# Performance work log

Measured on AMD Instinct MI355X. Metric: run time of the kernel, lower is better.

Reference implementation:

```python
import jax, jax.numpy as jnp
import numpy as np

N_NODES = 50000
N_EDGES = 800000
N_FEAT = 128
N_GRAPHS = 512
OUT_DIM = 128


def gcn_conv(x, W, b, src, dst, ew, n):
    """PyG GCNConv: h = x @ W; add self-loops (weight 1); symmetric norm
    D^-1/2 A D^-1/2 with edge weights; scatter-add messages src->dst; + bias."""
    h = x @ W  # [n, out]
    loop = jnp.arange(n)
    s = jnp.concatenate([src, loop])
    d = jnp.concatenate([dst, loop])
    w = jnp.concatenate([ew, jnp.ones((n,), x.dtype)])
    deg = jax.ops.segment_sum(w, d, num_segments=n)
    dinv = jnp.where(deg > 0, jax.lax.rsqrt(deg), 0.0)
    norm = dinv[s] * w * dinv[d]  # [E+n]
    out = jax.ops.segment_sum(h[s] * norm[:, None], d, num_segments=n)
    return out + b


def setup_inputs() -> dict:
    key = jax.random.key(0)
    ks = jax.random.split(key, 12)
    F = N_FEAT
    x = jax.random.normal(ks[0], (N_NODES, F), jnp.float32)
    edge_index = jax.random.randint(ks[1], (2, N_EDGES), 0, N_NODES, jnp.int64)
    edge_attr = jax.random.uniform(ks[2], (N_EDGES,), jnp.float32)
    # deterministic sorted graph assignment -> no empty graphs (avoids -inf in max pool)
    batch = (jnp.arange(N_NODES, dtype=jnp.int64) * N_GRAPHS) // N_NODES
    def lin(k, fi, fo):
        s = 1.0 / np.sqrt(fi)
        return jax.random.uniform(k, (fi, fo), jnp.float32, -s, s)
    return {
        "x": x, "edge_attr": edge_attr,
        "W1": lin(ks[3], F, F), "b1": jnp.zeros((F,), jnp.float32),
        "W2": lin(ks[4], F, 2 * F), "b2": jnp.zeros((2 * F,), jnp.float32),
        "W3": lin(ks[5], 2 * F, 4 * F), "b3": jnp.zeros((4 * F,), jnp.float32),
        "Wf1": lin(ks[6], 4 * F, 1024), "bf1": jnp.zeros((1024,), jnp.float32),
        "Wf2": lin(ks[7], 1024, OUT_DIM), "bf2": jnp.zeros((OUT_DIM,), jnp.float32),
        "edge_index": edge_index, "batch": batch,
    }


def reference(x, edge_attr, W1, b1, W2, b2, W3, b3, Wf1, bf1, Wf2, bf2,
              edge_index, batch):
    n = x.shape[0]
    src, dst = edge_index[0], edge_index[1]
    h = jax.nn.relu(gcn_conv(x, W1, b1, src, dst, edge_attr, n))
    h = jax.nn.relu(gcn_conv(h, W2, b2, src, dst, edge_attr, n))
    h = jax.nn.relu(gcn_conv(h, W3, b3, src, dst, edge_attr, n))
    # global max pool over nodes per graph
    g = jax.ops.segment_max(h, batch, num_segments=N_GRAPHS)  # [G, 4F]
    g = jax.nn.relu(g @ Wf1 + bf1)
    # dropout is identity in eval mode
    out = g @ Wf2 + bf2
    return out
```

## Files before the change

kernel.cpp:

```cpp
#include <hip/hip_runtime.h>

#define NNODES 50000
#define NPAD   50048
#define NEDGES 800000
#define NGRAPH 512
#define DCAP 64

typedef short bf16x8 __attribute__((ext_vector_type(8)));
typedef unsigned short u16x8 __attribute__((ext_vector_type(8)));
typedef float f32x4 __attribute__((ext_vector_type(4)));
typedef unsigned long long u64;

#define GLOAD16(g, l)                                                                 \
    __builtin_amdgcn_global_load_lds((const __attribute__((address_space(1))) unsigned*)(g), \
                                     (__attribute__((address_space(3))) unsigned*)(l), 16, 0, 0)

static __device__ __forceinline__ float b2f(unsigned short u) {
    return __uint_as_float(((unsigned)u) << 16);
}
static __device__ __forceinline__ unsigned short f2b(float f) {
    unsigned u = __float_as_uint(f);
    unsigned r = (u + 0x7fffu + ((u >> 16) & 1u)) >> 16;
    return (unsigned short)r;
}

static __device__ __forceinline__ void accum8(float (&acc)[8], float c, uint4 v) {
    unsigned w[4] = {v.x, v.y, v.z, v.w};
    #pragma unroll
    for (int i = 0; i < 4; ++i) {
        acc[2 * i]     += c * __uint_as_float(w[i] << 16);
        acc[2 * i + 1] += c * __uint_as_float(w[i] & 0xffff0000u);
    }
}

__global__ __launch_bounds__(256) void k_init(const float* __restrict__ W1, const float* __restrict__ W2,
                                              const float* __restrict__ W3, const float* __restrict__ Wf1,
                                              const float* __restrict__ Wf2,
                                              unsigned short* __restrict__ T1, unsigned short* __restrict__ T2,
                                              unsigned short* __restrict__ T3, unsigned short* __restrict__ Tf1,
                                              unsigned short* __restrict__ Tf2,
                                              u64* deg_cnt, int* gp) {
    int i = blockIdx.x * 256 + threadIdx.x;
    if (i < NNODES) deg_cnt[i] = (u64)(1u << 24);
    if (i < NGRAPH * 512) gp[i] = 0;

    const int b = blockIdx.x;
    if (b >= 204) return;
    const float* W; unsigned short* T; int K, N, t0;
    if (b < 4)        { W = W1;  T = T1;  K = 128;  N = 128;  t0 = 0;   }
    else if (b < 12)  { W = W2;  T = T2;  K = 128;  N = 256;  t0 = 4;   }
    else if (b < 44)  { W = W3;  T = T3;  K = 256;  N = 512;  t0 = 12;  }
    else if (b < 172) { W = Wf1; T = Tf1; K = 512;  N = 1024; t0 = 44;  }
    else              { W = Wf2; T = Tf2; K = 1024; N = 128;  t0 = 172; }
    const int tile = b - t0;
    const int ntn = N >> 6;
    const int k0 = (tile / ntn) * 64, n0 = (tile % ntn) * 64;
    __shared__ float sm[64][65];
    const int t = threadIdx.x;
    const int rr = t >> 6, cc = t & 63;
    #pragma unroll
    for (int r = 0; r < 16; ++r) {
        int kl = r * 4 + rr;
        sm[kl][cc] = W[(size_t)(k0 + kl) * N + n0 + cc];
    }
    __syncthreads();
    #pragma unroll
    for (int r = 0; r < 16; ++r) {
        int nl = r * 4 + rr;
        T[(size_t)(n0 + nl) * K + k0 + cc] = f2b(sm[cc][nl]);
    }
}

__global__ __launch_bounds__(256) void k_count(const int4* __restrict__ ei_s,
                                               const int4* __restrict__ ei_d,
                                               const float4* __restrict__ ew4,
                                               u64* deg_cnt,
                                               unsigned* __restrict__ edges) {
    int t = blockIdx.x * 256 + threadIdx.x;
    if (t >= NEDGES / 4) return;
    int4 ss = ei_s[t];
    int4 dd = ei_d[t];
    float4 ww = ew4[t];
    int s[4] = {ss.x, ss.y, ss.z, ss.w};
    int d[4] = {dd.x, dd.y, dd.z, dd.w};
    float w[4] = {ww.x, ww.y, ww.z, ww.w};
    int slot[4];
    #pragma unroll
    for (int u = 0; u < 4; ++u) {
        unsigned fixed = __float2uint_rn(w[u] * 16777216.0f);
        u64 old = atomicAdd(&deg_cnt[d[u]], ((u64)1 << 32) | fixed);
        slot[u] = (int)(old >> 32);
        if (slot[u] > DCAP - 1) slot[u] = DCAP - 1;
    }
    #pragma unroll
    for (int u = 0; u < 4; ++u)
        edges[((unsigned)d[u] << 6) | slot[u]] = ((unsigned)f2b(w[u]) << 16) | (unsigned)s[u];
}

__global__ void k_cvt_prep(const float* __restrict__ X, const u64* __restrict__ deg_cnt,
                           float* __restrict__ dinv, unsigned short* __restrict__ Y, int n4) {
    int i = blockIdx.x * 256 + threadIdx.x;
    if (i < n4) {
        int row = i >> 5;
        float d = rsqrtf((float)(unsigned)(deg_cnt[row] & 0xffffffffull) * 5.9604645e-8f);
        if ((i & 31) == 0) dinv[row] = d;
        float4 v = ((const float4*)X)[i];
        uint2 o;
        o.x = (unsigned)f2b(v.x * d) | ((unsigned)f2b(v.y * d) << 16);
        o.y = (unsigned)f2b(v.z * d) | ((unsigned)f2b(v.w * d) << 16);
        ((uint2*)Y)[i] = o;
    }
}

template <int F, int SLICES>
__global__ __launch_bounds__(256) void k_aggregate(const unsigned short* __restrict__ X,
                                                   const u64* __restrict__ deg_cnt,
                                                   const unsigned* __restrict__ edges,
                                                   const float* __restrict__ dinv,
                                                   unsigned short* __restrict__ Z) {
    constexpr int FS = F / SLICES;
    constexpr int LPR = FS / 8;
    constexpr int GRP = 64 / LPR;
    constexpr int STEP = GRP * 2;
    const int bid = blockIdx.x;
    const int slice = (SLICES == 1) ? 0 : (bid & (SLICES - 1));
    const int chunk = (SLICES == 1) ? bid : (bid / SLICES);
    const int wave = threadIdx.x >> 6, lane = threadIdx.x & 63;
    const int node = chunk * 4 + wave;
    if (node >= NNODES) return;
    const int sub = lane & (LPR - 1);
    const int grp = lane / LPR;
    const int fo = slice * FS + sub * 8;
    const unsigned short* Xf = X + fo;
    const float di = dinv[node];
    const int cnt = (int)(deg_cnt[node] >> 32);
    const unsigned* erow = edges + ((unsigned)node << 6);

    const uint4 selfv = *(const uint4*)(Xf + (size_t)node * F);

    float acc[8] = {};

    const int e0 = grp;
    const int nb = (cnt + STEP - 1) / STEP;

    unsigned pa0 = 0, pb0 = 0, pa1 = 0, pb1 = 0;
    uint4 va0 = {}, vb0 = {};
    if (nb > 0) {
        int ea = e0, eb = e0 + GRP;
        pa0 = (ea < cnt) ? erow[ea] : 0u;
        pb0 = (eb < cnt) ? erow[eb] : 0u;
        va0 = *(const uint4*)(Xf + (size_t)(pa0 & 0xffffu) * F);
        vb0 = *(const uint4*)(Xf + (size_t)(pb0 & 0xffffu) * F);
        if (nb > 1) {
            int ea1 = e0 + STEP, eb1 = ea1 + GRP;
            pa1 = (ea1 < cnt) ? erow[ea1] : 0u;
            pb1 = (eb1 < cnt) ? erow[eb1] : 0u;
        }
    }
    for (int p = 0; p < nb; ++p) {
        uint4 va1 = {}, vb1 = {};
        unsigned pa2 = 0, pb2 = 0;
        if (p + 1 < nb) {
            va1 = *(const uint4*)(Xf + (size_t)(pa1 & 0xffffu) * F);
            vb1 = *(const uint4*)(Xf + (size_t)(pb1 & 0xffffu) * F);
            if (p + 2 < nb) {
                int ea = e0 + (p + 2) * STEP, eb = ea + GRP;
                pa2 = (ea < cnt) ? erow[ea] : 0u;
                pb2 = (eb < cnt) ? erow[eb] : 0u;
            }
        }
        accum8(acc, b2f((unsigned short)(pa0 >> 16)), va0);
        accum8(acc, b2f((unsigned short)(pb0 >> 16)), vb0);
        pa0 = pa1; pb0 = pb1; va0 = va1; vb0 = vb1;
        pa1 = pa2; pb1 = pb2;
    }

    #pragma unroll
    for (int j = 0; j < 8; ++j) {
        if constexpr (GRP == 4) acc[j] += __shfl_xor(acc[j], 16, 64);
        acc[j] += __shfl_xor(acc[j], 32, 64);
    }

    if (grp == 0) {
        unsigned w[4] = {selfv.x, selfv.y, selfv.z, selfv.w};
        unsigned o[4];
        #pragma unroll
        for (int i = 0; i < 4; ++i) {
            float s0 = __uint_as_float(w[i] << 16);
            float s1 = __uint_as_float(w[i] & 0xffff0000u);
            unsigned short c0 = f2b(di * (acc[2 * i] + s0));
            unsigned short c1 = f2b(di * (acc[2 * i + 1] + s1));
            o[i] = (unsigned)c0 | ((unsigned)c1 << 16);
        }
        uint4 ov; ov.x = o[0]; ov.y = o[1]; ov.z = o[2]; ov.w = o[3];
        *(uint4*)(Z + (size_t)node * F + fo) = ov;
    }
}

template <int CMODE>
__global__ __launch_bounds__(256) void k_gemm128(const unsigned short* __restrict__ A,
                                                 const unsigned short* __restrict__ WT,
                                                 const float* __restrict__ bias,
                                                 unsigned short* __restrict__ C,
                                                 const int* __restrict__ batch,
                                                 int* __restrict__ gp,
                                                 const float* __restrict__ rscale,
                                                 int M, int N, int K) {
    __shared__ unsigned short As[2][128 * 32];
    __shared__ unsigned short Bs[2][128 * 32];
    const int tid = threadIdx.x;

    const int nwg = gridDim.x * gridDim.y;
    const int f = blockIdx.y * gridDim.x + blockIdx.x;
    const int q = nwg >> 3, r = nwg & 7;
    const int xcd = f & 7, idx = f >> 3;
    const int w = (xcd < r) ? xcd * (q + 1) + idx : r * (q + 1) + (xcd - r) * q + idx;
    const int m0 = (w / gridDim.x) * 128;
    const int n0 = (w % gridDim.x) * 128;

    const int wave = tid >> 6, lane = tid & 63;
    const int wm = (wave >> 1) * 64, wn = (wave & 1) * 64;
    const int quad = lane >> 4, mrow = lane & 15;

    const int sr = tid >> 2;
    const int sc = (tid & 3) * 8;
    const unsigned short* Ag0 = A + (size_t)(m0 + sr) * K + sc;
    const unsigned short* Ag1 = A + (size_t)(m0 + 64 + sr) * K + sc;
    const unsigned short* Bg0 = WT + (size_t)(n0 + sr) * K + sc;
    const unsigned short* Bg1 = WT + (size_t)(n0 + 64 + sr) * K + sc;
    const int so0 = sr * 32 + sc, so1 = (64 + sr) * 32 + sc;

    f32x4 acc[4][4] = {};
    const int nsteps = K >> 5;

    GLOAD16(Ag0, &As[0][so0]);
    GLOAD16(Ag1, &As[0][so1]);
    GLOAD16(Bg0, &Bs[0][so0]);
    GLOAD16(Bg1, &Bs[0][so1]);
    __syncthreads();

    for (int step = 0; step < nsteps; ++step) {
        const int cur = step & 1;
        if (step + 1 < nsteps) {
            const int k1 = (step + 1) << 5;
            GLOAD16(Ag0 + k1, &As[cur ^ 1][so0]);
            GLOAD16(Ag1 + k1, &As[cur ^ 1][so1]);
            GLOAD16(Bg0 + k1, &Bs[cur ^ 1][so0]);
            GLOAD16(Bg1 + k1, &Bs[cur ^ 1][so1]);
        }
        bf16x8 af[4], bf[4];
        #pragma unroll
        for (int mt = 0; mt < 4; ++mt)
            af[mt] = *(const bf16x8*)&As[cur][(wm + mt * 16 + mrow) * 32 + quad * 8];
        #pragma unroll
        for (int nt = 0; nt < 4; ++nt)
            bf[nt] = *(const bf16x8*)&Bs[cur][(wn + nt * 16 + mrow) * 32 + quad * 8];
        #pragma unroll
        for (int mt = 0; mt < 4; ++mt)
            #pragma unroll
            for (int nt = 0; nt < 4; ++nt)
                acc[mt][nt] = __builtin_amdgcn_mfma_f32_16x16x32_bf16(af[mt], bf[nt], acc[mt][nt], 0, 0, 0);
        __syncthreads();
    }

    float bn[4];
    #pragma unroll
    for (int nt = 0; nt < 4; ++nt) bn[nt] = bias[n0 + wn + nt * 16 + mrow];

    if constexpr (CMODE == 0) {
        #pragma unroll
        for (int mt = 0; mt < 4; ++mt) {
            #pragma unroll
            for (int r4 = 0; r4 < 4; ++r4) {
                int row = m0 + wm + mt * 16 + quad * 4 + r4;
                if (row < M) {
                    float rs = rscale ? rscale[row] : 1.0f;
                    #pragma unroll
                    for (int nt = 0; nt < 4; ++nt) {
                        float v = fmaxf(acc[mt][nt][r4] + bn[nt], 0.f) * rs;
                        C[(size_t)row * N + n0 + wn + nt * 16 + mrow] = f2b(v);
                    }
                }
            }
        }
    } else {
        const int wr0 = m0 + wm;
        int g0i = wr0 < M ? wr0 : M - 1;
        const int g0 = batch[g0i];
        int lastr = wr0 + 63; if (lastr >= M) lastr = M - 1;
        const int gl = batch[lastr];
        bool rok[16]; int gid[16];
        #pragma unroll
        for (int mt = 0; mt < 4; ++mt)
            #pragma unroll
            for (int r4 = 0; r4 < 4; ++r4) {
                int row = wr0 + mt * 16 + quad * 4 + r4;
                rok[mt * 4 + r4] = row < M;
                gid[mt * 4 + r4] = (row < M) ? batch[row] : -1;
            }
        #pragma unroll
        for (int nt = 0; nt < 4; ++nt) {
            float v0 = 0.f, v1 = 0.f;
            #pragma unroll
            for (int mt = 0; mt < 4; ++mt)
                #pragma unroll
                for (int r4 = 0; r4 < 4; ++r4)
                    if (rok[mt * 4 + r4]) {
                        float v = fmaxf(acc[mt][nt][r4] + bn[nt], 0.f);
                        if (gid[mt * 4 + r4] == g0) v0 = fmaxf(v0, v);
                        else v1 = fmaxf(v1, v);
                    }
            v0 = fmaxf(v0, __shfl_xor(v0, 16, 64));
            v0 = fmaxf(v0, __shfl_xor(v0, 32, 64));
            v1 = fmaxf(v1, __shfl_xor(v1, 16, 64));
            v1 = fmaxf(v1, __shfl_xor(v1, 32, 64));
            if (quad == 0) {
                int c = n0 + wn + nt * 16 + mrow;
                atomicMax(&gp[(size_t)g0 * N + c], __float_as_int(v0));
                if (gl != g0) atomicMax(&gp[(size_t)gl * N + c], __float_as_int(v1));
            }
        }
    }
}

template <int CMODE, int AFP>
__global__ __launch_bounds__(256) void k_gemm_mfma(const void* __restrict__ Av,
                                                   const unsigned short* __restrict__ WT,
                                                   const float* __restrict__ bias,
                                                   void* __restrict__ Cv,
                                                   int M, int N, int K) {
    constexpr int LDK = 40;
    __shared__ unsigned short As[64 * LDK];
    __shared__ unsigned short Bs[128 * LDK];
    const int tid = threadIdx.x;
    const int m0 = blockIdx.y * 64, n0 = blockIdx.x * 128;
    const int wave = tid >> 6, lane = tid & 63;
    const int wm = (wave >> 1) * 32;
    const int wn = (wave & 1) * 64;
    const int quad = lane >> 4, mrow = lane & 15;

    const int ar = tid >> 2;
    const int ak = (tid & 3) * 8;
    const bool arow_ok = (m0 + ar) < M;
    const size_t aoff = (size_t)(m0 + ar) * K + ak;
    const unsigned short* Bg0 = WT + (size_t)(n0 + ar) * K + ak;
    const unsigned short* Bg1 = WT + (size_t)(n0 + ar + 64) * K + ak;

    f32x4 acc[2][4] = {};

    for (int k0 = 0; k0 < K; k0 += 32) {
        u16x8 av = {};
        if (arow_ok) {
            if constexpr (AFP) {
                const float* Af = (const float*)Av + aoff + k0;
                float4 f0 = *(const float4*)Af;
                float4 f1 = *(const float4*)(Af + 4);
                av[0] = (short)f2b(f0.x); av[1] = (short)f2b(f0.y);
                av[2] = (short)f2b(f0.z); av[3] = (short)f2b(f0.w);
                av[4] = (short)f2b(f1.x); av[5] = (short)f2b(f1.y);
                av[6] = (short)f2b(f1.z); av[7] = (short)f2b(f1.w);
            } else {
                av = *(const u16x8*)((const unsigned short*)Av + aoff + k0);
            }
        }
        u16x8 bv0 = *(const u16x8*)(Bg0 + k0);
        u16x8 bv1 = *(const u16x8*)(Bg1 + k0);
        *(u16x8*)&As[ar * LDK + ak] = av;
        *(u16x8*)&Bs[ar * LDK + ak] = bv0;
        *(u16x8*)&Bs[(ar + 64) * LDK + ak] = bv1;
        __syncthreads();
        bf16x8 af[2], bf[4];
        #pragma unroll
        for (int mt = 0; mt < 2; ++mt)
            af[mt] = *(const bf16x8*)&As[(wm + mt * 16 + mrow) * LDK + quad * 8];
        #pragma unroll
        for (int nt = 0; nt < 4; ++nt)
            bf[nt] = *(const bf16x8*)&Bs[(wn + nt * 16 + mrow) * LDK + quad * 8];
        #pragma unroll
        for (int mt = 0; mt < 2; ++mt)
            #pragma unroll
            for (int nt = 0; nt < 4; ++nt)
                acc[mt][nt] = __builtin_amdgcn_mfma_f32_16x16x32_bf16(af[mt], bf[nt], acc[mt][nt], 0, 0, 0);
        __syncthreads();
    }

    float bn[4];
    #pragma unroll
    for (int nt = 0; nt < 4; ++nt) bn[nt] = bias[n0 + wn + nt * 16 + mrow];

    if constexpr (CMODE == 0) {
        unsigned short* C = (unsigned short*)Cv;
        #pragma unroll
        for (int mt = 0; mt < 2; ++mt) {
            #pragma unroll
            for (int r = 0; r < 4; ++r) {
                int row = m0 + wm + mt * 16 + quad * 4 + r;
                if (row < M) {
                    #pragma unroll
                    for (int nt = 0; nt < 4; ++nt) {
                        float v = fmaxf(acc[mt][nt][r] + bn[nt], 0.f);
                        C[(size_t)row * N + n0 + wn + nt * 16 + mrow] = f2b(v);
                    }
                }
            }
        }
    } else {
        float* C = (float*)Cv;
        #pragma unroll
        for (int mt = 0; mt < 2; ++mt) {
            #pragma unroll
            for (int r = 0; r < 4; ++r) {
                int row = m0 + wm + mt * 16 + quad * 4 + r;
                if (row < M) {
                    #pragma unroll
                    for (int nt = 0; nt < 4; ++nt)
                        C[(size_t)row * N + n0 + wn + nt * 16 + mrow] = acc[mt][nt][r] + bn[nt];
                }
            }
        }
    }
}

extern "C" void kernel_launch(void* const* d_in, const int* in_sizes, int n_in,
                              void* d_out, int out_size, void* d_ws, size_t ws_size,
                              hipStream_t stream) {
    const float* x   = (const float*)d_in[0];
    const float* ew  = (const float*)d_in[1];
    const float* W1  = (const float*)d_in[2];
    const float* b1  = (const float*)d_in[3];
    const float* W2  = (const float*)d_in[4];
    const float* b2  = (const float*)d_in[5];
    const float* W3  = (const float*)d_in[6];
    const float* b3  = (const float*)d_in[7];
    const float* Wf1 = (const float*)d_in[8];
    const float* bf1 = (const float*)d_in[9];
    const float* Wf2 = (const float*)d_in[10];
    const float* bf2 = (const float*)d_in[11];
    const int* ei    = (const int*)d_in[12];
    const int* batch = (const int*)d_in[13];
    float* out = (float*)d_out;
    (void)in_sizes; (void)n_in; (void)out_size; (void)ws_size;

    char* p = (char*)d_ws;
    auto alloc = [&](size_t bytes) -> char* {
        char* r = p;
        p += (bytes + 255) & ~(size_t)255;
        return r;
    };
    u64*   deg_cnt = (u64*)alloc((size_t)NNODES * 8);
    float* dinv   = (float*)alloc((size_t)NNODES * 4);
    unsigned* edges = (unsigned*)alloc((size_t)NNODES * DCAP * 4);
    int*   gp     = (int*)  alloc((size_t)NGRAPH * 512 * 4);
    unsigned short* f1   = (unsigned short*)alloc((size_t)NGRAPH * 1024 * 2);
    unsigned short* wt1  = (unsigned short*)alloc((size_t)128 * 128 * 2);
    unsigned short* wt2  = (unsigned short*)alloc((size_t)256 * 128 * 2);
    unsigned short* wt3  = (unsigned short*)alloc((size_t)512 * 256 * 2);
    unsigned short* wtf1 = (unsigned short*)alloc((size_t)1024 * 512 * 2);
    unsigned short* wtf2 = (unsigned short*)alloc((size_t)128 * 1024 * 2);
    unsigned short* bufA = (unsigned short*)alloc((size_t)NPAD * 256 * 2);
    unsigned short* bufB = (unsigned short*)alloc((size_t)NPAD * 256 * 2);
    unsigned short* x16  = bufB;

    const int MB128 = (NNODES + 127) / 128;
    const int AGG = (NNODES + 3) / 4;

    k_init<<<1024, 256, 0, stream>>>(W1, W2, W3, Wf1, Wf2,
                                     wt1, wt2, wt3, wtf1, wtf2, deg_cnt, gp);
    k_count<<<(NEDGES / 4 + 255) / 256, 256, 0, stream>>>(
        (const int4*)ei, (const int4*)(ei + NEDGES), (const float4*)ew, deg_cnt, edges);
    k_cvt_prep<<<(NNODES * 32 + 255) / 256, 256, 0, stream>>>(x, deg_cnt, dinv, x16, NNODES * 32);

    k_aggregate<128, 1><<<AGG, 256, 0, stream>>>(x16, deg_cnt, edges, dinv, bufA);
    k_gemm128<0><<<dim3(1, MB128), 256, 0, stream>>>(bufA, wt1, b1, bufB, nullptr, nullptr, dinv, NNODES, 128, 128);
    k_aggregate<128, 1><<<AGG, 256, 0, stream>>>(bufB, deg_cnt, edges, dinv, bufA);
    k_gemm128<0><<<dim3(2, MB128), 256, 0, stream>>>(bufA, wt2, b2, bufB, nullptr, nullptr, dinv, NNODES, 256, 128);
    k_aggregate<256, 2><<<AGG * 2, 256, 0, stream>>>(bufB, deg_cnt, edges, dinv, bufA);
    k_gemm128<2><<<dim3(4, MB128), 256, 0, stream>>>(bufA, wt3, b3, nullptr, batch, gp, nullptr, NNODES, 512, 256);

    k_gemm_mfma<0, 1><<<dim3(8, NGRAPH / 64), 256, 0, stream>>>(gp, wtf1, bf1, f1, NGRAPH, 1024, 512);
    k_gemm_mfma<1, 0><<<dim3(1, NGRAPH / 64), 256, 0, stream>>>(f1, wtf2, bf2, out, NGRAPH, 128, 1024);
}
```

Baseline: 363.6 us.

## Merge weight transpose and edge bucketing into one kernel, pad degree counters

```diff
diff --git a/kernel.cpp b/kernel.cpp
--- a/kernel.cpp
+++ b/kernel.cpp
@@ -33,68 +33,52 @@
     }
 }
 
-__global__ __launch_bounds__(256) void k_init(const float* __restrict__ W1, const float* __restrict__ W2,
-                                              const float* __restrict__ W3, const float* __restrict__ Wf1,
-                                              const float* __restrict__ Wf2,
-                                              unsigned short* __restrict__ T1, unsigned short* __restrict__ T2,
-                                              unsigned short* __restrict__ T3, unsigned short* __restrict__ Tf1,
-                                              unsigned short* __restrict__ Tf2,
-                                              u64* deg_cnt, int* gp) {
-    int i = blockIdx.x * 256 + threadIdx.x;
-    if (i < NNODES) deg_cnt[i] = (u64)(1u << 24);
-    if (i < NGRAPH * 512) gp[i] = 0;
-
+__global__ __launch_bounds__(256) void k_graph(const float* __restrict__ W1, const float* __restrict__ W2,
+                                               const float* __restrict__ W3, const float* __restrict__ Wf1,
+                                               const float* __restrict__ Wf2,
+                                               unsigned short* __restrict__ T1, unsigned short* __restrict__ T2,
+                                               unsigned short* __restrict__ T3, unsigned short* __restrict__ Tf1,
+                                               unsigned short* __restrict__ Tf2,
+                                               const int* __restrict__ ei_s, const int* __restrict__ ei_d,
+                                               const float* __restrict__ ew,
+                                               u64* deg_cnt, unsigned* __restrict__ edges) {
     const int b = blockIdx.x;
-    if (b >= 204) return;
-    const float* W; unsigned short* T; int K, N, t0;
-    if (b < 4)        { W = W1;  T = T1;  K = 128;  N = 128;  t0 = 0;   }
-    else if (b < 12)  { W = W2;  T = T2;  K = 128;  N = 256;  t0 = 4;   }
-    else if (b < 44)  { W = W3;  T = T3;  K = 256;  N = 512;  t0 = 12;  }
-    else if (b < 172) { W = Wf1; T = Tf1; K = 512;  N = 1024; t0 = 44;  }
-    else              { W = Wf2; T = Tf2; K = 1024; N = 128;  t0 = 172; }
-    const int tile = b - t0;
-    const int ntn = N >> 6;
-    const int k0 = (tile / ntn) * 64, n0 = (tile % ntn) * 64;
-    __shared__ float sm[64][65];
-    const int t = threadIdx.x;
-    const int rr = t >> 6, cc = t & 63;
-    #pragma unroll
-    for (int r = 0; r < 16; ++r) {
-        int kl = r * 4 + rr;
-        sm[kl][cc] = W[(size_t)(k0 + kl) * N + n0 + cc];
-    }
-    __syncthreads();
-    #pragma unroll
-    for (int r = 0; r < 16; ++r) {
-        int nl = r * 4 + rr;
-        T[(size_t)(n0 + nl) * K + k0 + cc] = f2b(sm[cc][nl]);
-    }
-}
-
-__global__ __launch_bounds__(256) void k_count(const int4* __restrict__ ei_s,
-                                               const int4* __restrict__ ei_d,
-                                               const float4* __restrict__ ew4,
-                                               u64* deg_cnt,
-                                               unsigned* __restrict__ edges) {
-    int t = blockIdx.x * 256 + threadIdx.x;
-    if (t >= NEDGES / 4) return;
-    int4 ss = ei_s[t];
-    int4 dd = ei_d[t];
-    float4 ww = ew4[t];
-    int s[4] = {ss.x, ss.y, ss.z, ss.w};
-    int d[4] = {dd.x, dd.y, dd.z, dd.w};
-    float w[4] = {ww.x, ww.y, ww.z, ww.w};
-    int slot[4];
-    #pragma unroll
-    for (int u = 0; u < 4; ++u) {
-        unsigned fixed = __float2uint_rn(w[u] * 16777216.0f);
-        u64 old = atomicAdd(&deg_cnt[d[u]], ((u64)1 << 32) | fixed);
-        slot[u] = (int)(old >> 32);
-        if (slot[u] > DCAP - 1) slot[u] = DCAP - 1;
-    }
-    #pragma unroll
-    for (int u = 0; u < 4; ++u)
-        edges[((unsigned)d[u] << 6) | slot[u]] = ((unsigned)f2b(w[u]) << 16) | (unsigned)s[u];
+    if (b < 204) {
+        const float* W; unsigned short* T; int K, N, t0;
+        if (b < 4)        { W = W1;  T = T1;  K = 128;  N = 128;  t0 = 0;   }
+        else if (b < 12)  { W = W2;  T = T2;  K = 128;  N = 256;  t0 = 4;   }
+        else if (b < 44)  { W = W3;  T = T3;  K = 256;  N = 512;  t0 = 12;  }
+        else if (b < 172) { W = Wf1; T = Tf1; K = 512;  N = 1024; t0 = 44;  }
+        else              { W = Wf2; T = Tf2; K = 1024; N = 128;  t0 = 172; }
+        const int tile = b - t0;
+        const int ntn = N >> 6;
+        const int k0 = (tile / ntn) * 64, n0 = (tile % ntn) * 64;
+        __shared__ float sm[64][65];
+        const int t = threadIdx.x;
+        const int rr = t >> 6, cc = t & 63;
+        #pragma unroll
+        for (int r = 0; r < 16; ++r) {
+            int kl = r * 4 + rr;
+            sm[kl][cc] = W[(size_t)(k0 + kl) * N + n0 + cc];
+        }
+        __syncthreads();
+        #pragma unroll
+        for (int r = 0; r < 16; ++r) {
+            int nl = r * 4 + rr;
+            T[(size_t)(n0 + nl) * K + k0 + cc] = f2b(sm[cc][nl]);
+        }
+        return;
+    }
+    const int e = (b - 204) * 256 + threadIdx.x;
+    if (e >= NEDGES) return;
+    const int s = ei_s[e];
+    const int d = ei_d[e];
+    const float w = ew[e];
+    const unsigned fixed = __float2uint_rn(w * 16777216.0f);
+    u64 old = atomicAdd(&deg_cnt[(size_t)d << 3], ((u64)1 << 32) | fixed);
+    int slot = (int)(old >> 32);
+    if (slot > DCAP - 1) slot = DCAP - 1;
+    edges[((unsigned)d << 6) | slot] = ((unsigned)f2b(w) << 16) | (unsigned)s;
 }
 
 __global__ void k_cvt_prep(const float* __restrict__ X, const u64* __restrict__ deg_cnt,
@@ -102,7 +86,7 @@
     int i = blockIdx.x * 256 + threadIdx.x;
     if (i < n4) {
         int row = i >> 5;
-        float d = rsqrtf((float)(unsigned)(deg_cnt[row] & 0xffffffffull) * 5.9604645e-8f);
+        float d = rsqrtf((float)(unsigned)(deg_cnt[(size_t)row << 3] & 0xffffffffull) * 5.9604645e-8f + 1.0f);
         if ((i & 31) == 0) dinv[row] = d;
         float4 v = ((const float4*)X)[i];
         uint2 o;
@@ -133,7 +117,7 @@
     const int fo = slice * FS + sub * 8;
     const unsigned short* Xf = X + fo;
     const float di = dinv[node];
-    const int cnt = (int)(deg_cnt[node] >> 32);
+    const int cnt = (int)(deg_cnt[(size_t)node << 3] >> 32);
     const unsigned* erow = edges + ((unsigned)node << 6);
 
     const uint4 selfv = *(const uint4*)(Xf + (size_t)node * F);
@@ -447,7 +431,7 @@
         p += (bytes + 255) & ~(size_t)255;
         return r;
     };
-    u64*   deg_cnt = (u64*)alloc((size_t)NNODES * 8);
+    u64*   deg_cnt = (u64*)alloc((size_t)NNODES * 64);
     float* dinv   = (float*)alloc((size_t)NNODES * 4);
     unsigned* edges = (unsigned*)alloc((size_t)NNODES * DCAP * 4);
     int*   gp     = (int*)  alloc((size_t)NGRAPH * 512 * 4);
@@ -463,11 +447,13 @@
 
     const int MB128 = (NNODES + 127) / 128;
     const int AGG = (NNODES + 3) / 4;
-
-    k_init<<<1024, 256, 0, stream>>>(W1, W2, W3, Wf1, Wf2,
-                                     wt1, wt2, wt3, wtf1, wtf2, deg_cnt, gp);
-    k_count<<<(NEDGES / 4 + 255) / 256, 256, 0, stream>>>(
-        (const int4*)ei, (const int4*)(ei + NEDGES), (const float4*)ew, deg_cnt, edges);
+    const int EB = (NEDGES + 255) / 256;
+
+    hipMemsetAsync(deg_cnt, 0, (size_t)NNODES * 64, stream);
+    hipMemsetAsync(gp, 0, (size_t)NGRAPH * 512 * 4, stream);
+    k_graph<<<204 + EB, 256, 0, stream>>>(W1, W2, W3, Wf1, Wf2,
+                                          wt1, wt2, wt3, wtf1, wtf2,
+                                          ei, ei + NEDGES, ew, deg_cnt, edges);
     k_cvt_prep<<<(NNODES * 32 + 255) / 256, 256, 0, stream>>>(x, deg_cnt, dinv, x16, NNODES * 32);
 
     k_aggregate<128, 1><<<AGG, 256, 0, stream>>>(x16, deg_cnt, edges, dinv, bufA);
```

Measured after the change: 377.0 us. 3.7% more time.

## Fuse edge counting, weight transpose and x conversion into one preprocessing launch

Applied to the files above, without the earlier changes.

```diff
diff --git a/kernel.cpp b/kernel.cpp
--- a/kernel.cpp
+++ b/kernel.cpp
@@ -33,86 +33,88 @@
     }
 }
 
-__global__ __launch_bounds__(256) void k_init(const float* __restrict__ W1, const float* __restrict__ W2,
-                                              const float* __restrict__ W3, const float* __restrict__ Wf1,
-                                              const float* __restrict__ Wf2,
-                                              unsigned short* __restrict__ T1, unsigned short* __restrict__ T2,
-                                              unsigned short* __restrict__ T3, unsigned short* __restrict__ Tf1,
-                                              unsigned short* __restrict__ Tf2,
-                                              u64* deg_cnt, int* gp) {
+#define EBLK 782
+__global__ __launch_bounds__(256) void k_pre(const float* __restrict__ W1, const float* __restrict__ W2,
+                                             const float* __restrict__ W3, const float* __restrict__ Wf1,
+                                             const float* __restrict__ Wf2,
+                                             unsigned short* __restrict__ T1, unsigned short* __restrict__ T2,
+                                             unsigned short* __restrict__ T3, unsigned short* __restrict__ Tf1,
+                                             unsigned short* __restrict__ Tf2,
+                                             const int4* __restrict__ ei_s, const int4* __restrict__ ei_d,
+                                             const float4* __restrict__ ew4,
+                                             u64* deg_cnt, unsigned* __restrict__ edges,
+                                             const float* __restrict__ x, unsigned short* __restrict__ x16) {
+    const int b = blockIdx.x;
+    if (b < EBLK) {
+        int t = b * 256 + threadIdx.x;
+        if (t >= NEDGES / 4) return;
+        int4 ss = ei_s[t];
+        int4 dd = ei_d[t];
+        float4 ww = ew4[t];
+        int s[4] = {ss.x, ss.y, ss.z, ss.w};
+        int d[4] = {dd.x, dd.y, dd.z, dd.w};
+        float w[4] = {ww.x, ww.y, ww.z, ww.w};
+        int slot[4];
+        #pragma unroll
+        for (int u = 0; u < 4; ++u) {
+            unsigned fixed = __float2uint_rn(w[u] * 16777216.0f);
+            u64 old = atomicAdd(&deg_cnt[d[u]], ((u64)1 << 32) | fixed);
+            slot[u] = (int)(old >> 32);
+            if (slot[u] > DCAP - 1) slot[u] = DCAP - 1;
+        }
+        #pragma unroll
+        for (int u = 0; u < 4; ++u)
+            edges[((unsigned)d[u] << 6) | slot[u]] = ((unsigned)f2b(w[u]) << 16) | (unsigned)s[u];
+        return;
+    }
+    if (b < EBLK + 204) {
+        const int bb = b - EBLK;
+        const float* W; unsigned short* T; int K, N, t0;
+        if (bb < 4)        { W = W1;  T = T1;  K = 128;  N = 128;  t0 = 0;   }
+        else if (bb < 12)  { W = W2;  T = T2;  K = 128;  N = 256;  t0 = 4;   }
+        else if (bb < 44)  { W = W3;  T = T3;  K = 256;  N = 512;  t0 = 12;  }
+        else if (bb < 172) { W = Wf1; T = Tf1; K = 512;  N = 1024; t0 = 44;  }
+        else               { W = Wf2; T = Tf2; K = 1024; N = 128;  t0 = 172; }
+        const int tile = bb - t0;
+        const int ntn = N >> 6;
+        const int k0 = (tile / ntn) * 64, n0 = (tile % ntn) * 64;
+        __shared__ float sm[64][65];
+        const int t = threadIdx.x;
+        const int rr = t >> 6, cc = t & 63;
+        #pragma unroll
+        for (int r = 0; r < 16; ++r) {
+            int kl = r * 4 + rr;
+            sm[kl][cc] = W[(size_t)(k0 + kl) * N + n0 + cc];
+        }
+        __syncthreads();
+        #pragma unroll
+        for (int r = 0; r < 16; ++r) {
+            int nl = r * 4 + rr;
+            T[(size_t)(n0 + nl) * K + k0 + cc] = f2b(sm[cc][nl]);
+        }
+        return;
+    }
+    int idx = (b - EBLK - 204) * 256 + threadIdx.x;
+    if (idx < NNODES * 16) {
+        float4 v0 = ((const float4*)x)[idx * 2];
+        float4 v1 = ((const float4*)x)[idx * 2 + 1];
+        uint4 o;
+        o.x = (unsigned)f2b(v0.x) | ((unsigned)f2b(v0.y) << 16);
+        o.y = (unsigned)f2b(v0.z) | ((unsigned)f2b(v0.w) << 16);
+        o.z = (unsigned)f2b(v1.x) | ((unsigned)f2b(v1.y) << 16);
+        o.w = (unsigned)f2b(v1.z) | ((unsigned)f2b(v1.w) << 16);
+        ((uint4*)x16)[idx] = o;
+    }
+}
+
+__global__ void k_prep(const u64* __restrict__ deg_cnt, float* __restrict__ dinv, int* __restrict__ gp) {
     int i = blockIdx.x * 256 + threadIdx.x;
-    if (i < NNODES) deg_cnt[i] = (u64)(1u << 24);
+    if (i < NNODES)
+        dinv[i] = rsqrtf((float)(unsigned)(deg_cnt[i] & 0xffffffffull) * 5.9604645e-8f + 1.0f);
     if (i < NGRAPH * 512) gp[i] = 0;
-
-    const int b = blockIdx.x;
-    if (b >= 204) return;
-    const float* W; unsigned short* T; int K, N, t0;
-    if (b < 4)        { W = W1;  T = T1;  K = 128;  N = 128;  t0 = 0;   }
-    else if (b < 12)  { W = W2;  T = T2;  K = 128;  N = 256;  t0 = 4;   }
-    else if (b < 44)  { W = W3;  T = T3;  K = 256;  N = 512;  t0 = 12;  }
-    else if (b < 172) { W = Wf1; T = Tf1; K = 512;  N = 1024; t0 = 44;  }
-    else              { W = Wf2; T = Tf2; K = 1024; N = 128;  t0 = 172; }
-    const int tile = b - t0;
-    const int ntn = N >> 6;
-    const int k0 = (tile / ntn) * 64, n0 = (tile % ntn) * 64;
-    __shared__ float sm[64][65];
-    const int t = threadIdx.x;
-    const int rr = t >> 6, cc = t & 63;
-    #pragma unroll
-    for (int r = 0; r < 16; ++r) {
-        int kl = r * 4 + rr;
-        sm[kl][cc] = W[(size_t)(k0 + kl) * N + n0 + cc];
-    }
-    __syncthreads();
-    #pragma unroll
-    for (int r = 0; r < 16; ++r) {
-        int nl = r * 4 + rr;
-        T[(size_t)(n0 + nl) * K + k0 + cc] = f2b(sm[cc][nl]);
-    }
-}
-
-__global__ __launch_bounds__(256) void k_count(const int4* __restrict__ ei_s,
-                                               const int4* __restrict__ ei_d,
-                                               const float4* __restrict__ ew4,
-                                               u64* deg_cnt,
-                                               unsigned* __restrict__ edges) {
-    int t = blockIdx.x * 256 + threadIdx.x;
-    if (t >= NEDGES / 4) return;
-    int4 ss = ei_s[t];
-    int4 dd = ei_d[t];
-    float4 ww = ew4[t];
-    int s[4] = {ss.x, ss.y, ss.z, ss.w};
-    int d[4] = {dd.x, dd.y, dd.z, dd.w};
-    float w[4] = {ww.x, ww.y, ww.z, ww.w};
-    int slot[4];
-    #pragma unroll
-    for (int u = 0; u < 4; ++u) {
-        unsigned fixed = __float2uint_rn(w[u] * 16777216.0f);
-        u64 old = atomicAdd(&deg_cnt[d[u]], ((u64)1 << 32) | fixed);
-        slot[u] = (int)(old >> 32);
-        if (slot[u] > DCAP - 1) slot[u] = DCAP - 1;
-    }
-    #pragma unroll
-    for (int u = 0; u < 4; ++u)
-        edges[((unsigned)d[u] << 6) | slot[u]] = ((unsigned)f2b(w[u]) << 16) | (unsigned)s[u];
-}
-
-__global__ void k_cvt_prep(const float* __restrict__ X, const u64* __restrict__ deg_cnt,
-                           float* __restrict__ dinv, unsigned short* __restrict__ Y, int n4) {
-    int i = blockIdx.x * 256 + threadIdx.x;
-    if (i < n4) {
-        int row = i >> 5;
-        float d = rsqrtf((float)(unsigned)(deg_cnt[row] & 0xffffffffull) * 5.9604645e-8f);
-        if ((i & 31) == 0) dinv[row] = d;
-        float4 v = ((const float4*)X)[i];
-        uint2 o;
-        o.x = (unsigned)f2b(v.x * d) | ((unsigned)f2b(v.y * d) << 16);
-        o.y = (unsigned)f2b(v.z * d) | ((unsigned)f2b(v.w * d) << 16);
-        ((uint2*)Y)[i] = o;
-    }
-}
-
-template <int F, int SLICES>
+}
+
+template <int F, int SLICES, bool DSRC>
 __global__ __launch_bounds__(256) void k_aggregate(const unsigned short* __restrict__ X,
                                                    const u64* __restrict__ deg_cnt,
                                                    const unsigned* __restrict__ edges,
@@ -145,12 +147,14 @@
 
     unsigned pa0 = 0, pb0 = 0, pa1 = 0, pb1 = 0;
     uint4 va0 = {}, vb0 = {};
+    float da0 = 1.f, db0 = 1.f;
     if (nb > 0) {
         int ea = e0, eb = e0 + GRP;
         pa0 = (ea < cnt) ? erow[ea] : 0u;
         pb0 = (eb < cnt) ? erow[eb] : 0u;
         va0 = *(const uint4*)(Xf + (size_t)(pa0 & 0xffffu) * F);
         vb0 = *(const uint4*)(Xf + (size_t)(pb0 & 0xffffu) * F);
+        if constexpr (DSRC) { da0 = dinv[pa0 & 0xffffu]; db0 = dinv[pb0 & 0xffffu]; }
         if (nb > 1) {
             int ea1 = e0 + STEP, eb1 = ea1 + GRP;
             pa1 = (ea1 < cnt) ? erow[ea1] : 0u;
@@ -159,19 +163,25 @@
     }
     for (int p = 0; p < nb; ++p) {
         uint4 va1 = {}, vb1 = {};
+        float da1 = 1.f, db1 = 1.f;
         unsigned pa2 = 0, pb2 = 0;
         if (p + 1 < nb) {
             va1 = *(const uint4*)(Xf + (size_t)(pa1 & 0xffffu) * F);
             vb1 = *(const uint4*)(Xf + (size_t)(pb1 & 0xffffu) * F);
+            if constexpr (DSRC) { da1 = dinv[pa1 & 0xffffu]; db1 = dinv[pb1 & 0xffffu]; }
             if (p + 2 < nb) {
                 int ea = e0 + (p + 2) * STEP, eb = ea + GRP;
                 pa2 = (ea < cnt) ? erow[ea] : 0u;
                 pb2 = (eb < cnt) ? erow[eb] : 0u;
             }
         }
-        accum8(acc, b2f((unsigned short)(pa0 >> 16)), va0);
-        accum8(acc, b2f((unsigned short)(pb0 >> 16)), vb0);
+        float ca = b2f((unsigned short)(pa0 >> 16));
+        float cb = b2f((unsigned short)(pb0 >> 16));
+        if constexpr (DSRC) { ca *= da0; cb *= db0; }
+        accum8(acc, ca, va0);
+        accum8(acc, cb, vb0);
         pa0 = pa1; pb0 = pb1; va0 = va1; vb0 = vb1;
+        da0 = da1; db0 = db1;
         pa1 = pa2; pb1 = pb2;
     }
 
@@ -182,14 +192,15 @@
     }
 
     if (grp == 0) {
+        const float sc = DSRC ? di : 1.0f;
         unsigned w[4] = {selfv.x, selfv.y, selfv.z, selfv.w};
         unsigned o[4];
         #pragma unroll
         for (int i = 0; i < 4; ++i) {
             float s0 = __uint_as_float(w[i] << 16);
             float s1 = __uint_as_float(w[i] & 0xffff0000u);
-            unsigned short c0 = f2b(di * (acc[2 * i] + s0));
-            unsigned short c1 = f2b(di * (acc[2 * i + 1] + s1));
+            unsigned short c0 = f2b(di * (acc[2 * i] + sc * s0));
+            unsigned short c1 = f2b(di * (acc[2 * i + 1] + sc * s1));
             o[i] = (unsigned)c0 | ((unsigned)c1 << 16);
         }
         uint4 ov; ov.x = o[0]; ov.y = o[1]; ov.z = o[2]; ov.w = o[3];
@@ -463,18 +474,20 @@
 
     const int MB128 = (NNODES + 127) / 128;
     const int AGG = (NNODES + 3) / 4;
-
-    k_init<<<1024, 256, 0, stream>>>(W1, W2, W3, Wf1, Wf2,
-                                     wt1, wt2, wt3, wtf1, wtf2, deg_cnt, gp);
-    k_count<<<(NEDGES / 4 + 255) / 256, 256, 0, stream>>>(
-        (const int4*)ei, (const int4*)(ei + NEDGES), (const float4*)ew, deg_cnt, edges);
-    k_cvt_prep<<<(NNODES * 32 + 255) / 256, 256, 0, stream>>>(x, deg_cnt, dinv, x16, NNODES * 32);
-
-    k_aggregate<128, 1><<<AGG, 256, 0, stream>>>(x16, deg_cnt, edges, dinv, bufA);
+    const int CVB = (NNODES * 16 + 255) / 256;
+
+    hipMemsetAsync(deg_cnt, 0, (size_t)NNODES * 8, stream);
+    k_pre<<<EBLK + 204 + CVB, 256, 0, stream>>>(W1, W2, W3, Wf1, Wf2,
+                                                wt1, wt2, wt3, wtf1, wtf2,
+                                                (const int4*)ei, (const int4*)(ei + NEDGES),
+                                                (const float4*)ew, deg_cnt, edges, x, x16);
+    k_prep<<<1024, 256, 0, stream>>>(deg_cnt, dinv, gp);
+
+    k_aggregate<128, 1, true><<<AGG, 256, 0, stream>>>(x16, deg_cnt, edges, dinv, bufA);
     k_gemm128<0><<<dim3(1, MB128), 256, 0, stream>>>(bufA, wt1, b1, bufB, nullptr, nullptr, dinv, NNODES, 128, 128);
-    k_aggregate<128, 1><<<AGG, 256, 0, stream>>>(bufB, deg_cnt, edges, dinv, bufA);
+    k_aggregate<128, 1, false><<<AGG, 256, 0, stream>>>(bufB, deg_cnt, edges, dinv, bufA);
     k_gemm128<0><<<dim3(2, MB128), 256, 0, stream>>>(bufA, wt2, b2, bufB, nullptr, nullptr, dinv, NNODES, 256, 128);
-    k_aggregate<256, 2><<<AGG * 2, 256, 0, stream>>>(bufB, deg_cnt, edges, dinv, bufA);
+    k_aggregate<256, 2, false><<<AGG * 2, 256, 0, stream>>>(bufB, deg_cnt, edges, dinv, bufA);
     k_gemm128<2><<<dim3(4, MB128), 256, 0, stream>>>(bufA, wt3, b3, nullptr, batch, gp, nullptr, NNODES, 512, 256);
 
     k_gemm_mfma<0, 1><<<dim3(8, NGRAPH / 64), 256, 0, stream>>>(gp, wtf1, bf1, f1, NGRAPH, 1024, 512);
```

After: 364.9 us. About the same (+0.4%).
